# Optimization experiments

Measured on AMD Instinct MI355X. Metric: run time of the kernel, lower is better.

Reference implementation:

```python
import jax, jax.numpy as jnp
import numpy as np

N, M, D = 16384, 8192, 3
ATOM_DIMS, CHEM, K = 6, 16, 16
GAMMA = 1.0
BIG = 1e10


def _leaky(x):
    return jax.nn.leaky_relu(x, negative_slope=0.2)


def _linear(x, W, b=None):
    # torch nn.Linear: y = x @ W.T + b, W: [out, in]
    y = x @ W.T
    return y if b is None else y + b


def setup_inputs() -> dict:
    key = jax.random.key(0)
    ks = jax.random.split(key, 16)

    def lin(k, out_d, in_d):
        bound = 1.0 / np.sqrt(in_d)
        k1, k2 = jax.random.split(k)
        W = jax.random.uniform(k1, (out_d, in_d), minval=-bound, maxval=bound, dtype=jnp.float32)
        b = jax.random.uniform(k2, (out_d,), minval=-bound, maxval=bound, dtype=jnp.float32)
        return W, b

    W_t1, b_t1 = lin(ks[0], CHEM, ATOM_DIMS)
    W_t2, b_t2 = lin(ks[1], CHEM, CHEM)
    W_t3, b_t3 = lin(ks[2], CHEM, CHEM)
    W_att = jax.random.uniform(ks[3], (1, K), minval=-1.0 / np.sqrt(K), maxval=1.0 / np.sqrt(K), dtype=jnp.float32)
    W_e1, b_e1 = lin(ks[4], CHEM, CHEM)
    W_e2, b_e2 = lin(ks[5], CHEM, CHEM)
    W_e3, b_e3 = lin(ks[6], CHEM, CHEM)

    return {
        "xyz": jax.random.normal(ks[7], (N, D), dtype=jnp.float32) * 10.0,
        "atom_xyz": jax.random.normal(ks[8], (M, D), dtype=jnp.float32) * 10.0,
        "atomtypes": jax.random.uniform(ks[9], (M, ATOM_DIMS), dtype=jnp.float32),
        "batch": jnp.zeros((N,), dtype=jnp.int64),
        "atom_batch": jnp.zeros((M,), dtype=jnp.int64),
        "W_t1": W_t1, "b_t1": b_t1, "W_t2": W_t2, "b_t2": b_t2, "W_t3": W_t3, "b_t3": b_t3,
        "W_att": W_att,
        "W_e1": W_e1, "b_e1": b_e1, "W_e2": W_e2, "b_e2": b_e2, "W_e3": W_e3, "b_e3": b_e3,
    }


def reference(xyz, atom_xyz, atomtypes, batch, atom_batch,
              W_t1, b_t1, W_t2, b_t2, W_t3, b_t3, W_att,
              W_e1, b_e1, W_e2, b_e2, W_e3, b_e3):
    # transform_types MLP on atom one-hots -> [M, CHEM]
    t = atomtypes[:, :ATOM_DIMS]
    t = _leaky(_linear(t, W_t1, b_t1))
    t = _leaky(_linear(t, W_t2, b_t2))
    t = _leaky(_linear(t, W_t3, b_t3))

    # batched kNN: squared distances [N, M], cross-batch pairs masked out
    d2 = (jnp.sum(xyz * xyz, -1)[:, None] + jnp.sum(atom_xyz * atom_xyz, -1)[None, :]
          - 2.0 * (xyz @ atom_xyz.T))
    d2 = jnp.where(batch[:, None] == atom_batch[None, :], d2, BIG)
    _, idx = jax.lax.top_k(-d2, K)  # idx: [N, K] nearest atoms

    x_ik = atom_xyz[idx]                       # [N, K, 3]
    vecs = xyz[:, None, :] - x_ik              # [N, K, 3]
    dists = jnp.sum(vecs * vecs, -1)           # [N, K]
    w = jnp.power(dists + 1e-8, -(1.0 + GAMMA) / 2.0)
    norm_vec = vecs * w[:, :, None]            # [N, K, 3]
    feat = t[idx]                              # [N, K, CHEM]

    # outer product [N, K, 3, C] transposed to [N, C, 3, K], attention Linear over K,
    # fused into one einsum (dropout is identity at eval)
    fx = jnp.einsum('nkd,nkc,k->ncd', norm_vec, feat, W_att[0])  # [N, C, 3]
    fx = jnp.sqrt(jnp.sum(fx * fx, -1))        # [N, C]

    fx = _leaky(_linear(fx, W_e1, b_e1))
    fx = _leaky(_linear(fx, W_e2, b_e2))
    fx = _linear(fx, W_e3, b_e3)
    return fx
```

## Files before the change

### kernel.cpp

```cpp
#include <hip/hip_runtime.h>
#include <cfloat>

#define NPTS   16384
#define MATOMS 8192
#define CH     16
#define ADIM   6
#define KNN    16
#define GROUPS_PER_BLOCK 8
#define PTSPG  2
#define BIGF   1e10f
#define SLOTS  16
#define CHUNK  512
#define NCHUNK (MATOMS/CHUNK)
#define VMINC  4
#define NPASS  (VMINC + NCHUNK)

#define OFF_POS4  0u
#define OFF_TBUF  131072u
#define OFF_ABAT  655360u
#define OFF_GSEG  688128u
#define GSEG_BYTES ((size_t)NPTS * SLOTS * 32 * 2)
#define WS_NEED_G (OFF_GSEG + GSEG_BYTES)

__device__ __forceinline__ float leakyf(float x) { return x >= 0.0f ? x : 0.2f * x; }

__global__ void __launch_bounds__(256) prep_kernel(
    const float* __restrict__ atom_xyz,
    const float* __restrict__ atomtypes,
    const int*   __restrict__ atom_batch,
    const float* __restrict__ Wt1, const float* __restrict__ bt1,
    const float* __restrict__ Wt2, const float* __restrict__ bt2,
    const float* __restrict__ Wt3, const float* __restrict__ bt3,
    float4* __restrict__ pos4,
    float*  __restrict__ tbuf,
    int*    __restrict__ abatch)
{
    __shared__ float w1[CH*ADIM], w2[CH*CH], w3[CH*CH], bb1[CH], bb2[CH], bb3[CH];
    const int tid = threadIdx.x;
    if (tid < CH*ADIM) w1[tid] = Wt1[tid];
    if (tid < CH*CH)   { w2[tid] = Wt2[tid]; w3[tid] = Wt3[tid]; }
    if (tid < CH)      { bb1[tid] = bt1[tid]; bb2[tid] = bt2[tid]; bb3[tid] = bt3[tid]; }
    __syncthreads();
    const int m = blockIdx.x * 256 + tid;
    if (m >= MATOMS) return;

    float x[ADIM];
    #pragma unroll
    for (int j = 0; j < ADIM; ++j) x[j] = atomtypes[m*ADIM + j];

    float h0[CH], h1[CH], h2[CH];
    #pragma unroll
    for (int c = 0; c < CH; ++c) {
        float a = 0.0f;
        #pragma unroll
        for (int j = 0; j < ADIM; ++j) a = fmaf(w1[c*ADIM+j], x[j], a);
        h0[c] = leakyf(a + bb1[c]);
    }
    #pragma unroll
    for (int c = 0; c < CH; ++c) {
        float a = 0.0f;
        #pragma unroll
        for (int j = 0; j < CH; ++j) a = fmaf(w2[c*CH+j], h0[j], a);
        h1[c] = leakyf(a + bb2[c]);
    }
    #pragma unroll
    for (int c = 0; c < CH; ++c) {
        float a = 0.0f;
        #pragma unroll
        for (int j = 0; j < CH; ++j) a = fmaf(w3[c*CH+j], h1[j], a);
        h2[c] = leakyf(a + bb3[c]);
    }
    #pragma unroll
    for (int c = 0; c < CH; ++c) tbuf[m*CH + c] = h2[c];

    const float ax = atom_xyz[m*3+0], ay = atom_xyz[m*3+1], az = atom_xyz[m*3+2];
    const float a2 = __fadd_rn(__fadd_rn(__fmul_rn(ax,ax), __fmul_rn(ay,ay)), __fmul_rn(az,az));
    pos4[m] = make_float4(ax, ay, az, a2);
    abatch[m] = atom_batch[m];
}

__device__ __forceinline__ void knn_tail(
    int c32, float px, float py, float pz, float pn2, int pb,
    int skip, int cnt, const unsigned short* seg,
    const float4* __restrict__ pos4, const int* __restrict__ abatch,
    int* idxk)
{
    int ovf = skip | (cnt > SLOTS);
    ovf |= __shfl_xor(ovf, 1);
    ovf |= __shfl_xor(ovf, 2);
    ovf |= __shfl_xor(ovf, 4);
    ovf |= __shfl_xor(ovf, 8);
    ovf |= __shfl_xor(ovf, 16);

    float bd[KNN]; int bi[KNN];
    #pragma unroll
    for (int j = 0; j < KNN; ++j) { bd[j] = FLT_MAX; bi[j] = 0x7fffffff; }

    if (ovf) {
        for (int t = 0; t < MATOMS/32; ++t) {
            const int i = t*32 + c32;
            const float4 a = pos4[i];
            const int ab = abatch[i];
            const float dot = fmaf(pz, a.z, fmaf(py, a.y, __fmul_rn(px, a.x)));
            float d2 = __fsub_rn(__fadd_rn(pn2, a.w), 2.0f * dot);
            d2 = (ab == pb) ? d2 : BIGF;
            if (d2 < bd[KNN-1]) {
                float d = d2; int id = i;
                #pragma unroll
                for (int j = 0; j < KNN; ++j) {
                    const bool sw = d < bd[j];
                    const float od = bd[j]; const int oi = bi[j];
                    bd[j] = sw ? d  : bd[j];
                    bi[j] = sw ? id : bi[j];
                    d  = sw ? od : d;
                    id = sw ? oi : id;
                }
            }
        }
    } else {
        for (int s = 0; s < cnt; ++s) {
            const int i = (int)seg[s*32];
            const float4 a = pos4[i];
            const float dot = fmaf(pz, a.z, fmaf(py, a.y, __fmul_rn(px, a.x)));
            const float d2 = __fsub_rn(__fadd_rn(pn2, a.w), 2.0f * dot);
            if (abatch[i] == pb && d2 <= bd[KNN-1]) {
                float d = d2; int id = i;
                #pragma unroll
                for (int j = 0; j < KNN; ++j) {
                    const bool sw = (d < bd[j]) || (d == bd[j] && id < bi[j]);
                    const float od = bd[j]; const int oi = bi[j];
                    bd[j] = sw ? d  : bd[j];
                    bi[j] = sw ? id : bi[j];
                    d  = sw ? od : d;
                    id = sw ? oi : id;
                }
            }
        }
    }

    #pragma unroll
    for (int k = 0; k < KNN; ++k) {
        float d = bd[0]; int i = bi[0];
        #pragma unroll
        for (int m = 1; m <= 16; m <<= 1) {
            const float pd = __shfl_xor(d, m);
            const int   pi = __shfl_xor(i, m);
            const bool take = (pd < d) || (pd == d && pi < i);
            d = take ? pd : d;
            i = take ? pi : i;
        }
        idxk[k] = i;
        const bool win = (bd[0] == d) && (bi[0] == i);
        if (win) {
            #pragma unroll
            for (int j = 0; j < KNN-1; ++j) { bd[j] = bd[j+1]; bi[j] = bi[j+1]; }
            bd[KNN-1] = FLT_MAX; bi[KNN-1] = 0x7fffffff;
        }
    }
}

template <int SEG_GLOBAL>
__global__ void __launch_bounds__(256) atom_main_tpl(
    const float* __restrict__ xyz,
    const int*   __restrict__ batch,
    const float4* __restrict__ pos4,
    const float* __restrict__ tbuf,
    const int*   __restrict__ abatch,
    unsigned short* __restrict__ gseg,
    const float* __restrict__ Watt,
    const float* __restrict__ We1, const float* __restrict__ be1,
    const float* __restrict__ We2, const float* __restrict__ be2,
    const float* __restrict__ We3, const float* __restrict__ be3,
    float* __restrict__ out)
{
    __shared__ float lw1t[CH*CH], lw2t[CH*CH], lw3t[CH*CH];
    __shared__ float lb1[CH], lb2[CH], lb3[CH], lwatt[KNN];
    __shared__ unsigned short lbuf[SEG_GLOBAL ? 1 : GROUPS_PER_BLOCK*PTSPG*SLOTS*32];
    __shared__ float4 lpos[2][CHUNK];
    const int tid = threadIdx.x;
    lw1t[tid] = We1[(tid & 15)*CH + (tid >> 4)];
    lw2t[tid] = We2[(tid & 15)*CH + (tid >> 4)];
    lw3t[tid] = We3[(tid & 15)*CH + (tid >> 4)];
    if (tid < CH) { lb1[tid] = be1[tid]; lb2[tid] = be2[tid]; lb3[tid] = be3[tid]; lwatt[tid] = Watt[tid]; }

    const int c32 = tid & 31;
    const int grp = tid >> 5;
    const int n0  = (blockIdx.x * GROUPS_PER_BLOCK + grp) * PTSPG;
    const int n1  = n0 + 1;

    const float px0 = xyz[n0*3+0], py0 = xyz[n0*3+1], pz0 = xyz[n0*3+2];
    const float px1 = xyz[n1*3+0], py1 = xyz[n1*3+1], pz1 = xyz[n1*3+2];
    const float pn20 = __fadd_rn(__fadd_rn(__fmul_rn(px0,px0), __fmul_rn(py0,py0)), __fmul_rn(pz0,pz0));
    const float pn21 = __fadd_rn(__fadd_rn(__fmul_rn(px1,px1), __fmul_rn(py1,py1)), __fmul_rn(pz1,pz1));
    const int pb0 = batch[n0];
    const int pb1 = batch[n1];

    {
        const float4 q0 = pos4[tid];
        const float4 q1 = pos4[tid+256];
        lpos[0][tid]     = make_float4(-2.0f*q0.x, -2.0f*q0.y, -2.0f*q0.z, q0.w);
        lpos[0][tid+256] = make_float4(-2.0f*q1.x, -2.0f*q1.y, -2.0f*q1.z, q1.w);
    }

    float vmin0 = FLT_MAX, vmin1 = FLT_MAX;
    float tauf0 = 0.0f, tauf1 = 0.0f;
    int   skip0 = 0, skip1 = 0;
    int   cnt0 = 0, cnt1 = 0;
    unsigned short* seg0;
    unsigned short* seg1;
    if (SEG_GLOBAL) {
        seg0 = gseg + (size_t)n0 * (SLOTS*32) + c32;
        seg1 = gseg + (size_t)n1 * (SLOTS*32) + c32;
    } else {
        seg0 = &lbuf[(grp*PTSPG + 0) * (SLOTS*32) + c32];
        seg1 = &lbuf[(grp*PTSPG + 1) * (SLOTS*32) + c32];
    }

    for (int g = 0; g < NPASS; ++g) {
        const int cur = g & 1;
        __syncthreads();
        float4 q0, q1;
        const bool pf = (g+1 < NPASS);
        if (pf) {
            const int nc = (g+1 < VMINC) ? (g+1) : (g+1-VMINC);
            const int base = nc*CHUNK;
            q0 = pos4[base+tid]; q1 = pos4[base+tid+256];
        }
        if (g == VMINC) {
            float tau0 = FLT_MAX, tau1 = FLT_MAX;
            {
                float v = vmin0;
                #pragma unroll
                for (int k = 0; k < KNN; ++k) {
                    float d = v;
                    d = fminf(d, __shfl_xor(d, 1));
                    d = fminf(d, __shfl_xor(d, 2));
                    d = fminf(d, __shfl_xor(d, 4));
                    d = fminf(d, __shfl_xor(d, 8));
                    d = fminf(d, __shfl_xor(d, 16));
                    tau0 = d;
                    if (v == d) v = FLT_MAX;
                }
            }
            {
                float v = vmin1;
                #pragma unroll
                for (int k = 0; k < KNN; ++k) {
                    float d = v;
                    d = fminf(d, __shfl_xor(d, 1));
                    d = fminf(d, __shfl_xor(d, 2));
                    d = fminf(d, __shfl_xor(d, 4));
                    d = fminf(d, __shfl_xor(d, 8));
                    d = fminf(d, __shfl_xor(d, 16));
                    tau1 = d;
                    if (v == d) v = FLT_MAX;
                }
            }
            skip0 = !(tau0 < BIGF);
            skip1 = !(tau1 < BIGF);
            tauf0 = skip0 ? -FLT_MAX : tau0 + (1e-5f*(fabsf(pn20) + fabsf(tau0)) + 1e-2f);
            tauf1 = skip1 ? -FLT_MAX : tau1 + (1e-5f*(fabsf(pn21) + fabsf(tau1)) + 1e-2f);
        }
        if (g < VMINC) {
            #pragma unroll 4
            for (int t = 0; t < CHUNK/32; ++t) {
                const int il = t*32 + c32;
                const float4 a = lpos[cur][il];
                const float lhs0 = fmaf(pz0, a.z, fmaf(py0, a.y, fmaf(px0, a.x, a.w)));
                const float lhs1 = fmaf(pz1, a.z, fmaf(py1, a.y, fmaf(px1, a.x, a.w)));
                if (lhs0 < vmin0) { if (abatch[g*CHUNK + il] == pb0) vmin0 = lhs0; }
                if (lhs1 < vmin1) { if (abatch[g*CHUNK + il] == pb1) vmin1 = lhs1; }
            }
        } else {
            const int cb = g - VMINC;
            #pragma unroll 4
            for (int t = 0; t < CHUNK/32; ++t) {
                const int il = t*32 + c32;
                const float4 a = lpos[cur][il];
                const float lhs0 = fmaf(pz0, a.z, fmaf(py0, a.y, fmaf(px0, a.x, a.w)));
                const float lhs1 = fmaf(pz1, a.z, fmaf(py1, a.y, fmaf(px1, a.x, a.w)));
                const int gi = cb*CHUNK + il;
                if (lhs0 <= tauf0) {
                    if (cnt0 < SLOTS) seg0[cnt0*32] = (unsigned short)gi;
                    ++cnt0;
                }
                if (lhs1 <= tauf1) {
                    if (cnt1 < SLOTS) seg1[cnt1*32] = (unsigned short)gi;
                    ++cnt1;
                }
            }
        }
        if (pf) {
            lpos[cur^1][tid]     = make_float4(-2.0f*q0.x, -2.0f*q0.y, -2.0f*q0.z, q0.w);
            lpos[cur^1][tid+256] = make_float4(-2.0f*q1.x, -2.0f*q1.y, -2.0f*q1.z, q1.w);
        }
    }

    int idxk0[KNN], idxk1[KNN];
    knn_tail(c32, px0, py0, pz0, pn20, pb0, skip0, cnt0, seg0, pos4, abatch, idxk0);
    knn_tail(c32, px1, py1, pz1, pn21, pb1, skip1, cnt1, seg1, pos4, abatch, idxk1);

    {
        const int half = (tid >> 4) & 1;
        const int c = tid & 15;
        const int myn = half ? n1 : n0;
        const float px = half ? px1 : px0;
        const float py = half ? py1 : py0;
        const float pz = half ? pz1 : pz0;
        int myidx[KNN];
        #pragma unroll
        for (int k = 0; k < KNN; ++k) myidx[k] = half ? idxk1[k] : idxk0[k];

        float ac0 = 0.0f, ac1 = 0.0f, ac2 = 0.0f;
        #pragma unroll
        for (int k = 0; k < KNN; ++k) {
            const int j = myidx[k];
            const float4 a = pos4[j];
            const float v0 = __fsub_rn(px, a.x);
            const float v1 = __fsub_rn(py, a.y);
            const float v2 = __fsub_rn(pz, a.z);
            const float dist = __fadd_rn(__fadd_rn(__fmul_rn(v0,v0), __fmul_rn(v1,v1)), __fmul_rn(v2,v2));
            const float w = 1.0f / __fadd_rn(dist, 1e-8f);
            const float nv0 = __fmul_rn(v0, w);
            const float nv1 = __fmul_rn(v1, w);
            const float nv2 = __fmul_rn(v2, w);
            const float fc = tbuf[(size_t)j * CH + c];
            const float fw = __fmul_rn(fc, lwatt[k]);
            ac0 = fmaf(nv0, fw, ac0);
            ac1 = fmaf(nv1, fw, ac1);
            ac2 = fmaf(nv2, fw, ac2);
        }
        const float s = __fadd_rn(__fadd_rn(__fmul_rn(ac0,ac0), __fmul_rn(ac1,ac1)),
                                  __fmul_rn(ac2,ac2));
        const float fx = sqrtf(s);

        float a1 = 0.0f;
        #pragma unroll
        for (int j = 0; j < CH; ++j) {
            const float fj = __shfl(fx, j, 16);
            a1 = fmaf(lw1t[j*CH + c], fj, a1);
        }
        const float g1 = leakyf(a1 + lb1[c]);

        float a2 = 0.0f;
        #pragma unroll
        for (int j = 0; j < CH; ++j) {
            const float gj = __shfl(g1, j, 16);
            a2 = fmaf(lw2t[j*CH + c], gj, a2);
        }
        const float g2 = leakyf(a2 + lb2[c]);

        float a3 = 0.0f;
        #pragma unroll
        for (int j = 0; j < CH; ++j) {
            const float gj = __shfl(g2, j, 16);
            a3 = fmaf(lw3t[j*CH + c], gj, a3);
        }
        out[(size_t)myn*CH + c] = a3 + lb3[c];
    }
}

extern "C" void kernel_launch(void* const* d_in, const int* in_sizes, int n_in,
                              void* d_out, int out_size, void* d_ws, size_t ws_size,
                              hipStream_t stream)
{
    (void)in_sizes; (void)n_in; (void)out_size;
    const float* xyz        = (const float*)d_in[0];
    const float* atom_xyz   = (const float*)d_in[1];
    const float* atomtypes  = (const float*)d_in[2];
    const int*   batch      = (const int*)d_in[3];
    const int*   atom_batch = (const int*)d_in[4];
    const float* Wt1 = (const float*)d_in[5];
    const float* bt1 = (const float*)d_in[6];
    const float* Wt2 = (const float*)d_in[7];
    const float* bt2 = (const float*)d_in[8];
    const float* Wt3 = (const float*)d_in[9];
    const float* bt3 = (const float*)d_in[10];
    const float* Watt = (const float*)d_in[11];
    const float* We1 = (const float*)d_in[12];
    const float* be1 = (const float*)d_in[13];
    const float* We2 = (const float*)d_in[14];
    const float* be2 = (const float*)d_in[15];
    const float* We3 = (const float*)d_in[16];
    const float* be3 = (const float*)d_in[17];

    char* ws = (char*)d_ws;
    float4* pos4  = (float4*)(ws + OFF_POS4);
    float*  tbuf  = (float*)(ws + OFF_TBUF);
    int*    abat  = (int*)(ws + OFF_ABAT);
    float*  out   = (float*)d_out;

    hipLaunchKernelGGL(prep_kernel, dim3(MATOMS/256), dim3(256), 0, stream,
                       atom_xyz, atomtypes, atom_batch,
                       Wt1, bt1, Wt2, bt2, Wt3, bt3,
                       pos4, tbuf, abat);

    if (ws_size >= WS_NEED_G) {
        unsigned short* gseg = (unsigned short*)(ws + OFF_GSEG);
        hipLaunchKernelGGL((atom_main_tpl<1>), dim3(NPTS/(GROUPS_PER_BLOCK*PTSPG)), dim3(256), 0, stream,
                           xyz, batch, pos4, tbuf, abat, gseg,
                           Watt, We1, be1, We2, be2, We3, be3,
                           out);
    } else {
        hipLaunchKernelGGL((atom_main_tpl<0>), dim3(NPTS/(GROUPS_PER_BLOCK*PTSPG)), dim3(256), 0, stream,
                           xyz, batch, pos4, tbuf, abat, (unsigned short*)nullptr,
                           Watt, We1, be1, We2, be2, We3, be3,
                           out);
    }
}
```

Before: 125.6 us.

## Use 64-lane groups per point pair and split kNN tail across wave halves

Each group of two query points now spans a full 64-lane wavefront instead of 32 lanes, so the chunk scans and candidate slots are spread over twice as many lanes and there are half as many points per block. The final kNN tail no longer runs serially for both points in every lane: each 32-lane half handles one point and merges its own and its partner half's candidate segments. This removes the duplicated per-point tail work. In exchange the grid doubles, SLOTS per lane drops to 12, and the overflow fallback, which scans all atoms, may trigger more often.

```diff
diff --git a/kernel.cpp b/kernel.cpp
--- a/kernel.cpp
+++ b/kernel.cpp
@@ -6,10 +6,10 @@
 #define CH     16
 #define ADIM   6
 #define KNN    16
-#define GROUPS_PER_BLOCK 8
+#define GRPS   4
 #define PTSPG  2
 #define BIGF   1e10f
-#define SLOTS  16
+#define SLOTS  12
 #define CHUNK  512
 #define NCHUNK (MATOMS/CHUNK)
 #define VMINC  4
@@ -19,7 +19,7 @@
 #define OFF_TBUF  131072u
 #define OFF_ABAT  655360u
 #define OFF_GSEG  688128u
-#define GSEG_BYTES ((size_t)NPTS * SLOTS * 32 * 2)
+#define GSEG_BYTES ((size_t)NPTS * SLOTS * 64 * 2)
 #define WS_NEED_G (OFF_GSEG + GSEG_BYTES)
 
 __device__ __forceinline__ float leakyf(float x) { return x >= 0.0f ? x : 0.2f * x; }
@@ -79,86 +79,6 @@
     abatch[m] = atom_batch[m];
 }
 
-__device__ __forceinline__ void knn_tail(
-    int c32, float px, float py, float pz, float pn2, int pb,
-    int skip, int cnt, const unsigned short* seg,
-    const float4* __restrict__ pos4, const int* __restrict__ abatch,
-    int* idxk)
-{
-    int ovf = skip | (cnt > SLOTS);
-    ovf |= __shfl_xor(ovf, 1);
-    ovf |= __shfl_xor(ovf, 2);
-    ovf |= __shfl_xor(ovf, 4);
-    ovf |= __shfl_xor(ovf, 8);
-    ovf |= __shfl_xor(ovf, 16);
-
-    float bd[KNN]; int bi[KNN];
-    #pragma unroll
-    for (int j = 0; j < KNN; ++j) { bd[j] = FLT_MAX; bi[j] = 0x7fffffff; }
-
-    if (ovf) {
-        for (int t = 0; t < MATOMS/32; ++t) {
-            const int i = t*32 + c32;
-            const float4 a = pos4[i];
-            const int ab = abatch[i];
-            const float dot = fmaf(pz, a.z, fmaf(py, a.y, __fmul_rn(px, a.x)));
-            float d2 = __fsub_rn(__fadd_rn(pn2, a.w), 2.0f * dot);
-            d2 = (ab == pb) ? d2 : BIGF;
-            if (d2 < bd[KNN-1]) {
-                float d = d2; int id = i;
-                #pragma unroll
-                for (int j = 0; j < KNN; ++j) {
-                    const bool sw = d < bd[j];
-                    const float od = bd[j]; const int oi = bi[j];
-                    bd[j] = sw ? d  : bd[j];
-                    bi[j] = sw ? id : bi[j];
-                    d  = sw ? od : d;
-                    id = sw ? oi : id;
-                }
-            }
-        }
-    } else {
-        for (int s = 0; s < cnt; ++s) {
-            const int i = (int)seg[s*32];
-            const float4 a = pos4[i];
-            const float dot = fmaf(pz, a.z, fmaf(py, a.y, __fmul_rn(px, a.x)));
-            const float d2 = __fsub_rn(__fadd_rn(pn2, a.w), 2.0f * dot);
-            if (abatch[i] == pb && d2 <= bd[KNN-1]) {
-                float d = d2; int id = i;
-                #pragma unroll
-                for (int j = 0; j < KNN; ++j) {
-                    const bool sw = (d < bd[j]) || (d == bd[j] && id < bi[j]);
-                    const float od = bd[j]; const int oi = bi[j];
-                    bd[j] = sw ? d  : bd[j];
-                    bi[j] = sw ? id : bi[j];
-                    d  = sw ? od : d;
-                    id = sw ? oi : id;
-                }
-            }
-        }
-    }
-
-    #pragma unroll
-    for (int k = 0; k < KNN; ++k) {
-        float d = bd[0]; int i = bi[0];
-        #pragma unroll
-        for (int m = 1; m <= 16; m <<= 1) {
-            const float pd = __shfl_xor(d, m);
-            const int   pi = __shfl_xor(i, m);
-            const bool take = (pd < d) || (pd == d && pi < i);
-            d = take ? pd : d;
-            i = take ? pi : i;
-        }
-        idxk[k] = i;
-        const bool win = (bd[0] == d) && (bi[0] == i);
-        if (win) {
-            #pragma unroll
-            for (int j = 0; j < KNN-1; ++j) { bd[j] = bd[j+1]; bi[j] = bi[j+1]; }
-            bd[KNN-1] = FLT_MAX; bi[KNN-1] = 0x7fffffff;
-        }
-    }
-}
-
 template <int SEG_GLOBAL>
 __global__ void __launch_bounds__(256) atom_main_tpl(
     const float* __restrict__ xyz,
@@ -175,7 +95,7 @@
 {
     __shared__ float lw1t[CH*CH], lw2t[CH*CH], lw3t[CH*CH];
     __shared__ float lb1[CH], lb2[CH], lb3[CH], lwatt[KNN];
-    __shared__ unsigned short lbuf[SEG_GLOBAL ? 1 : GROUPS_PER_BLOCK*PTSPG*SLOTS*32];
+    __shared__ unsigned short lbuf[SEG_GLOBAL ? 1 : GRPS*PTSPG*SLOTS*64];
     __shared__ float4 lpos[2][CHUNK];
     const int tid = threadIdx.x;
     lw1t[tid] = We1[(tid & 15)*CH + (tid >> 4)];
@@ -183,9 +103,9 @@
     lw3t[tid] = We3[(tid & 15)*CH + (tid >> 4)];
     if (tid < CH) { lb1[tid] = be1[tid]; lb2[tid] = be2[tid]; lb3[tid] = be3[tid]; lwatt[tid] = Watt[tid]; }
 
-    const int c32 = tid & 31;
-    const int grp = tid >> 5;
-    const int n0  = (blockIdx.x * GROUPS_PER_BLOCK + grp) * PTSPG;
+    const int c64 = tid & 63;
+    const int grp = tid >> 6;
+    const int n0  = (blockIdx.x * GRPS + grp) * PTSPG;
     const int n1  = n0 + 1;
 
     const float px0 = xyz[n0*3+0], py0 = xyz[n0*3+1], pz0 = xyz[n0*3+2];
@@ -209,11 +129,11 @@
     unsigned short* seg0;
     unsigned short* seg1;
     if (SEG_GLOBAL) {
-        seg0 = gseg + (size_t)n0 * (SLOTS*32) + c32;
-        seg1 = gseg + (size_t)n1 * (SLOTS*32) + c32;
+        seg0 = gseg + (size_t)n0 * (SLOTS*64) + c64;
+        seg1 = gseg + (size_t)n1 * (SLOTS*64) + c64;
     } else {
-        seg0 = &lbuf[(grp*PTSPG + 0) * (SLOTS*32) + c32];
-        seg1 = &lbuf[(grp*PTSPG + 1) * (SLOTS*32) + c32];
+        seg0 = &lbuf[(grp*PTSPG + 0) * (SLOTS*64) + c64];
+        seg1 = &lbuf[(grp*PTSPG + 1) * (SLOTS*64) + c64];
     }
 
     for (int g = 0; g < NPASS; ++g) {
@@ -227,44 +147,34 @@
             q0 = pos4[base+tid]; q1 = pos4[base+tid+256];
         }
         if (g == VMINC) {
-            float tau0 = FLT_MAX, tau1 = FLT_MAX;
-            {
-                float v = vmin0;
-                #pragma unroll
-                for (int k = 0; k < KNN; ++k) {
-                    float d = v;
-                    d = fminf(d, __shfl_xor(d, 1));
-                    d = fminf(d, __shfl_xor(d, 2));
-                    d = fminf(d, __shfl_xor(d, 4));
-                    d = fminf(d, __shfl_xor(d, 8));
-                    d = fminf(d, __shfl_xor(d, 16));
-                    tau0 = d;
-                    if (v == d) v = FLT_MAX;
-                }
-            }
-            {
-                float v = vmin1;
-                #pragma unroll
-                for (int k = 0; k < KNN; ++k) {
-                    float d = v;
-                    d = fminf(d, __shfl_xor(d, 1));
-                    d = fminf(d, __shfl_xor(d, 2));
-                    d = fminf(d, __shfl_xor(d, 4));
-                    d = fminf(d, __shfl_xor(d, 8));
-                    d = fminf(d, __shfl_xor(d, 16));
-                    tau1 = d;
-                    if (v == d) v = FLT_MAX;
-                }
-            }
+            const float v0f = fminf(vmin0, __shfl_xor(vmin0, 32));
+            const float v1f = fminf(vmin1, __shfl_xor(vmin1, 32));
+            const int half = c64 >> 5;
+            float v = half ? v1f : v0f;
+            float tauh = FLT_MAX;
+            #pragma unroll
+            for (int k = 0; k < KNN; ++k) {
+                float d = v;
+                d = fminf(d, __shfl_xor(d, 1));
+                d = fminf(d, __shfl_xor(d, 2));
+                d = fminf(d, __shfl_xor(d, 4));
+                d = fminf(d, __shfl_xor(d, 8));
+                d = fminf(d, __shfl_xor(d, 16));
+                tauh = d;
+                if (v == d) v = FLT_MAX;
+            }
+            const float tauo = __shfl_xor(tauh, 32);
+            const float tau0 = half ? tauo : tauh;
+            const float tau1 = half ? tauh : tauo;
             skip0 = !(tau0 < BIGF);
             skip1 = !(tau1 < BIGF);
             tauf0 = skip0 ? -FLT_MAX : tau0 + (1e-5f*(fabsf(pn20) + fabsf(tau0)) + 1e-2f);
             tauf1 = skip1 ? -FLT_MAX : tau1 + (1e-5f*(fabsf(pn21) + fabsf(tau1)) + 1e-2f);
         }
         if (g < VMINC) {
-            #pragma unroll 4
-            for (int t = 0; t < CHUNK/32; ++t) {
-                const int il = t*32 + c32;
+            #pragma unroll
+            for (int t = 0; t < CHUNK/64; ++t) {
+                const int il = t*64 + c64;
                 const float4 a = lpos[cur][il];
                 const float lhs0 = fmaf(pz0, a.z, fmaf(py0, a.y, fmaf(px0, a.x, a.w)));
                 const float lhs1 = fmaf(pz1, a.z, fmaf(py1, a.y, fmaf(px1, a.x, a.w)));
@@ -273,19 +183,19 @@
             }
         } else {
             const int cb = g - VMINC;
-            #pragma unroll 4
-            for (int t = 0; t < CHUNK/32; ++t) {
-                const int il = t*32 + c32;
+            #pragma unroll
+            for (int t = 0; t < CHUNK/64; ++t) {
+                const int il = t*64 + c64;
                 const float4 a = lpos[cur][il];
                 const float lhs0 = fmaf(pz0, a.z, fmaf(py0, a.y, fmaf(px0, a.x, a.w)));
                 const float lhs1 = fmaf(pz1, a.z, fmaf(py1, a.y, fmaf(px1, a.x, a.w)));
                 const int gi = cb*CHUNK + il;
                 if (lhs0 <= tauf0) {
-                    if (cnt0 < SLOTS) seg0[cnt0*32] = (unsigned short)gi;
+                    if (cnt0 < SLOTS) seg0[cnt0*64] = (unsigned short)gi;
                     ++cnt0;
                 }
                 if (lhs1 <= tauf1) {
-                    if (cnt1 < SLOTS) seg1[cnt1*32] = (unsigned short)gi;
+                    if (cnt1 < SLOTS) seg1[cnt1*64] = (unsigned short)gi;
                     ++cnt1;
                 }
             }
@@ -296,29 +206,142 @@
         }
     }
 
-    int idxk0[KNN], idxk1[KNN];
-    knn_tail(c32, px0, py0, pz0, pn20, pb0, skip0, cnt0, seg0, pos4, abatch, idxk0);
-    knn_tail(c32, px1, py1, pz1, pn21, pb1, skip1, cnt1, seg1, pos4, abatch, idxk1);
-
-    {
-        const int half = (tid >> 4) & 1;
-        const int c = tid & 15;
+    int ovf0 = skip0 | (cnt0 > SLOTS);
+    ovf0 |= __shfl_xor(ovf0, 1);
+    ovf0 |= __shfl_xor(ovf0, 2);
+    ovf0 |= __shfl_xor(ovf0, 4);
+    ovf0 |= __shfl_xor(ovf0, 8);
+    ovf0 |= __shfl_xor(ovf0, 16);
+    ovf0 |= __shfl_xor(ovf0, 32);
+    int ovf1 = skip1 | (cnt1 > SLOTS);
+    ovf1 |= __shfl_xor(ovf1, 1);
+    ovf1 |= __shfl_xor(ovf1, 2);
+    ovf1 |= __shfl_xor(ovf1, 4);
+    ovf1 |= __shfl_xor(ovf1, 8);
+    ovf1 |= __shfl_xor(ovf1, 16);
+    ovf1 |= __shfl_xor(ovf1, 32);
+    const int cnt0p = __shfl_xor(cnt0, 32);
+    const int cnt1p = __shfl_xor(cnt1, 32);
+
+    const int half = c64 >> 5;
+    const int hl   = c64 & 31;
+    const float mpx = half ? px1 : px0;
+    const float mpy = half ? py1 : py0;
+    const float mpz = half ? pz1 : pz0;
+    const float mpn2 = half ? pn21 : pn20;
+    const int   mpb  = half ? pb1 : pb0;
+    const int   movf = half ? ovf1 : ovf0;
+    const int   mcA  = half ? cnt1  : cnt0;
+    const int   mcB  = half ? cnt1p : cnt0p;
+    const unsigned short* msegA;
+    const unsigned short* msegB;
+    if (SEG_GLOBAL) {
+        const unsigned short* base = gseg + (size_t)(half ? n1 : n0) * (SLOTS*64);
+        msegA = base + c64;
+        msegB = base + (c64 ^ 32);
+    } else {
+        const unsigned short* base = &lbuf[(grp*PTSPG + half) * (SLOTS*64)];
+        msegA = base + c64;
+        msegB = base + (c64 ^ 32);
+    }
+
+    float bd[KNN]; int bi[KNN];
+    #pragma unroll
+    for (int j = 0; j < KNN; ++j) { bd[j] = FLT_MAX; bi[j] = 0x7fffffff; }
+
+    if (movf) {
+        for (int t = 0; t < MATOMS/32; ++t) {
+            const int i = t*32 + hl;
+            const float4 a = pos4[i];
+            const int ab = abatch[i];
+            const float dot = fmaf(mpz, a.z, fmaf(mpy, a.y, __fmul_rn(mpx, a.x)));
+            float d2 = __fsub_rn(__fadd_rn(mpn2, a.w), 2.0f * dot);
+            d2 = (ab == mpb) ? d2 : BIGF;
+            if (d2 < bd[KNN-1]) {
+                float d = d2; int id = i;
+                #pragma unroll
+                for (int j = 0; j < KNN; ++j) {
+                    const bool sw = d < bd[j];
+                    const float od = bd[j]; const int oi = bi[j];
+                    bd[j] = sw ? d  : bd[j];
+                    bi[j] = sw ? id : bi[j];
+                    d  = sw ? od : d;
+                    id = sw ? oi : id;
+                }
+            }
+        }
+    } else {
+        for (int s = 0; s < mcA; ++s) {
+            const int i = (int)msegA[s*64];
+            const float4 a = pos4[i];
+            const float dot = fmaf(mpz, a.z, fmaf(mpy, a.y, __fmul_rn(mpx, a.x)));
+            const float d2 = __fsub_rn(__fadd_rn(mpn2, a.w), 2.0f * dot);
+            if (abatch[i] == mpb && d2 <= bd[KNN-1]) {
+                float d = d2; int id = i;
+                #pragma unroll
+                for (int j = 0; j < KNN; ++j) {
+                    const bool sw = (d < bd[j]) || (d == bd[j] && id < bi[j]);
+                    const float od = bd[j]; const int oi = bi[j];
+                    bd[j] = sw ? d  : bd[j];
+                    bi[j] = sw ? id : bi[j];
+                    d  = sw ? od : d;
+                    id = sw ? oi : id;
+                }
+            }
+        }
+        for (int s = 0; s < mcB; ++s) {
+            const int i = (int)msegB[s*64];
+            const float4 a = pos4[i];
+            const float dot = fmaf(mpz, a.z, fmaf(mpy, a.y, __fmul_rn(mpx, a.x)));
+            const float d2 = __fsub_rn(__fadd_rn(mpn2, a.w), 2.0f * dot);
+            if (abatch[i] == mpb && d2 <= bd[KNN-1]) {
+                float d = d2; int id = i;
+                #pragma unroll
+                for (int j = 0; j < KNN; ++j) {
+                    const bool sw = (d < bd[j]) || (d == bd[j] && id < bi[j]);
+                    const float od = bd[j]; const int oi = bi[j];
+                    bd[j] = sw ? d  : bd[j];
+                    bi[j] = sw ? id : bi[j];
+                    d  = sw ? od : d;
+                    id = sw ? oi : id;
+                }
+            }
+        }
+    }
+
+    int idxk[KNN];
+    #pragma unroll
+    for (int k = 0; k < KNN; ++k) {
+        float d = bd[0]; int i = bi[0];
+        #pragma unroll
+        for (int m = 1; m <= 16; m <<= 1) {
+            const float pd = __shfl_xor(d, m);
+            const int   pi = __shfl_xor(i, m);
+            const bool take = (pd < d) || (pd == d && pi < i);
+            d = take ? pd : d;
+            i = take ? pi : i;
+        }
+        idxk[k] = i;
+        const bool win = (bd[0] == d) && (bi[0] == i);
+        if (win) {
+            #pragma unroll
+            for (int j = 0; j < KNN-1; ++j) { bd[j] = bd[j+1]; bi[j] = bi[j+1]; }
+            bd[KNN-1] = FLT_MAX; bi[KNN-1] = 0x7fffffff;
+        }
+    }
+
+    if ((c64 & 16) == 0) {
+        const int c = c64 & 15;
         const int myn = half ? n1 : n0;
-        const float px = half ? px1 : px0;
-        const float py = half ? py1 : py0;
-        const float pz = half ? pz1 : pz0;
-        int myidx[KNN];
-        #pragma unroll
-        for (int k = 0; k < KNN; ++k) myidx[k] = half ? idxk1[k] : idxk0[k];
 
         float ac0 = 0.0f, ac1 = 0.0f, ac2 = 0.0f;
         #pragma unroll
         for (int k = 0; k < KNN; ++k) {
-            const int j = myidx[k];
+            const int j = idxk[k];
             const float4 a = pos4[j];
-            const float v0 = __fsub_rn(px, a.x);
-            const float v1 = __fsub_rn(py, a.y);
-            const float v2 = __fsub_rn(pz, a.z);
+            const float v0 = __fsub_rn(mpx, a.x);
+            const float v1 = __fsub_rn(mpy, a.y);
+            const float v2 = __fsub_rn(mpz, a.z);
             const float dist = __fadd_rn(__fadd_rn(__fmul_rn(v0,v0), __fmul_rn(v1,v1)), __fmul_rn(v2,v2));
             const float w = 1.0f / __fadd_rn(dist, 1e-8f);
             const float nv0 = __fmul_rn(v0, w);
@@ -397,12 +420,12 @@
 
     if (ws_size >= WS_NEED_G) {
         unsigned short* gseg = (unsigned short*)(ws + OFF_GSEG);
-        hipLaunchKernelGGL((atom_main_tpl<1>), dim3(NPTS/(GROUPS_PER_BLOCK*PTSPG)), dim3(256), 0, stream,
+        hipLaunchKernelGGL((atom_main_tpl<1>), dim3(NPTS/(GRPS*PTSPG)), dim3(256), 0, stream,
                            xyz, batch, pos4, tbuf, abat, gseg,
                            Watt, We1, be1, We2, be2, We3, be3,
                            out);
     } else {
-        hipLaunchKernelGGL((atom_main_tpl<0>), dim3(NPTS/(GROUPS_PER_BLOCK*PTSPG)), dim3(256), 0, stream,
+        hipLaunchKernelGGL((atom_main_tpl<0>), dim3(NPTS/(GRPS*PTSPG)), dim3(256), 0, stream,
                            xyz, batch, pos4, tbuf, abat, (unsigned short*)nullptr,
                            Watt, We1, be1, We2, be2, We3, be3,
                            out);
```

After: 137.3 us. +9.3%, slower.
